# Kernel optimization log

Measured on AMD Instinct MI355X. Metric: run time of the kernel, lower is better.

Reference implementation:

```python
import jax, jax.numpy as jnp
import numpy as np

EPS = 1e-7
B, N, DIM, NH, HD, WIN, HASH_WIN = 2, 1024, 512, 8, 64, 64, 8


def expmap0(v, c):
    sqrt_c = jnp.clip(jnp.sqrt(c), EPS)
    v_norm = jnp.linalg.norm(v, axis=-1, keepdims=True)
    is_zero = v_norm < EPS
    safe = jnp.clip(v_norm, EPS)
    mag = jnp.tanh(sqrt_c * safe) / sqrt_c
    return jnp.where(is_zero, jnp.zeros_like(v), mag * (v / safe))


def poincare_dist(x, y, c):
    # x: (B,H,N,1,D), y: (B,H,N,W,D), c: (B,1,1,1,1) -> (B,H,N,W)
    sqrt_c = jnp.clip(jnp.sqrt(c), EPS)
    x2 = jnp.sum(x * x, -1, keepdims=True)
    y2 = jnp.sum(y * y, -1, keepdims=True)
    xy = jnp.sum(x * y, -1, keepdims=True)
    num = (1 - 2 * c * xy + c * y2) * x + (1 - c * x2) * (-y)
    den = 1 - 2 * c * xy + c * c * x2 * y2
    diff = num / jnp.clip(den, EPS)
    dn = jnp.linalg.norm(diff, axis=-1)
    arg = jnp.minimum(jnp.squeeze(sqrt_c, -1) * jnp.clip(dn, EPS), 1.0 - EPS)
    return 2.0 * jnp.arctanh(arg) / jnp.squeeze(sqrt_c, -1)


def sliding_windows(t, w):
    # t: (B,H,N,D) -> (B,H,N,w,D), left-padded causal window
    Bb, H, Nn, D = t.shape
    pad = jnp.zeros((Bb, H, w - 1, D), t.dtype)
    tp = jnp.concatenate([pad, t], axis=2)
    idx = jnp.arange(w)[None, :] + jnp.arange(Nn)[:, None]  # (N,w)
    return tp[:, :, idx, :]


def layernorm(x, s, b):
    m = jnp.mean(x, -1, keepdims=True)
    v = jnp.var(x, -1, keepdims=True)
    return (x - m) / jnp.sqrt(v + 1e-6) * s + b


def rope(x, cos, sin):
    # x: (B,N,H,hd), cos/sin: (N, hd//2) -- complex rotation in real arithmetic
    xr, xi = jnp.split(x, 2, axis=-1)
    cos = cos[None, :, None, :]
    sin = sin[None, :, None, :]
    return jnp.concatenate([xr * cos - xi * sin, xr * sin + xi * cos], axis=-1)


def setup_inputs() -> dict:
    key = jax.random.key(0)
    ks = jax.random.split(key, 10)
    x = jax.random.normal(ks[0], (B, N, DIM), jnp.float32)
    pos = jnp.arange(N, dtype=jnp.float32)
    inv = 1.0 / (10000.0 ** (jnp.arange(0, HD, 2, dtype=jnp.float32) / HD))
    ang = pos[:, None] * inv[None, :]  # (N, HD//2)
    freqs_cos, freqs_sin = jnp.cos(ang), jnp.sin(ang)
    c = jax.random.uniform(ks[1], (B,), jnp.float32) * 0.9 + 0.1
    s = 0.02
    Wq = jax.random.normal(ks[2], (DIM, DIM), jnp.float32) * s
    Wk = jax.random.normal(ks[3], (DIM, DIM), jnp.float32) * s
    Wv = jax.random.normal(ks[4], (DIM, DIM), jnp.float32) * s
    Wo = jax.random.normal(ks[5], (DIM, DIM), jnp.float32) * s
    W1 = jax.random.normal(ks[6], (DIM, 4 * DIM), jnp.float32) * s
    W2 = jax.random.normal(ks[7], (4 * DIM, DIM), jnp.float32) * s
    bq = jnp.zeros((DIM,)); bk = jnp.zeros((DIM,)); bv = jnp.zeros((DIM,))
    bo = jnp.zeros((DIM,)); b1 = jnp.zeros((4 * DIM,)); b2 = jnp.zeros((DIM,))
    ln1_s = jnp.ones((DIM,)); ln1_b = jnp.zeros((DIM,))
    ln2_s = jnp.ones((DIM,)); ln2_b = jnp.zeros((DIM,))
    geo_scale = jnp.ones((NH, 1, 1), jnp.float32)
    hash_offset = jax.random.normal(ks[8], (1, 1, NH, HD), jnp.float32) * 0.01
    return dict(x=x, freqs_cos=freqs_cos, freqs_sin=freqs_sin, c=c,
                Wq=Wq, bq=bq, Wk=Wk, bk=bk, Wv=Wv, bv=bv, Wo=Wo, bo=bo,
                W1=W1, b1=b1, W2=W2, b2=b2,
                ln1_s=ln1_s, ln1_b=ln1_b, ln2_s=ln2_s, ln2_b=ln2_b,
                geo_scale=geo_scale, hash_offset=hash_offset)


def reference(x, freqs_cos, freqs_sin, c, Wq, bq, Wk, bk, Wv, bv, Wo, bo,
              W1, b1, W2, b2, ln1_s, ln1_b, ln2_s, ln2_b, geo_scale, hash_offset):
    x_res = x
    xn = layernorm(x, ln1_s, ln1_b)
    q = (xn @ Wq + bq).reshape(B, N, NH, HD)
    k = (xn @ Wk + bk).reshape(B, N, NH, HD)
    v = (xn @ Wv + bv).reshape(B, N, NH, HD)
    q = q + hash_offset * jnp.log(1.0 + HASH_WIN)
    q_rot = rope(q, freqs_cos, freqs_sin)
    k_rot = rope(k, freqs_cos, freqs_sin)
    c_b = c.reshape(B, 1, 1, 1)
    q_h = expmap0(q_rot, c_b)
    k_h = expmap0(k_rot, c_b)
    q_h, k_h, v = (t.transpose(0, 2, 1, 3) for t in (q_h, k_h, v))  # (B,H,N,D)
    k_win = sliding_windows(k_h, WIN)  # (B,H,N,W,D)
    v_win = sliding_windows(v, WIN)
    dist = poincare_dist(q_h[:, :, :, None, :], k_win, c.reshape(B, 1, 1, 1, 1))  # (B,H,N,W)
    scores = -geo_scale * dist
    w = jax.nn.softmax(scores, axis=-1)
    attn = jnp.einsum('bhnw,bhnwd->bhnd', w, v_win)
    attn = attn.transpose(0, 2, 1, 3).reshape(B, N, DIM)
    x_out = x_res + (attn @ Wo + bo)
    h = layernorm(x_out, ln2_s, ln2_b)
    ffn = jax.nn.gelu(h @ W1 + b1) @ W2 + b2
    return x_out + ffn
```

## Files before the change

kernel.cpp:

```cpp
#include <hip/hip_runtime.h>
#include <math.h>
#include <stdint.h>

#define Bn   2
#define Nn   1024
#define DIMn 512
#define NHn  8
#define HDn  64
#define QKVS 1536
#define EPSF 1e-7f

typedef __attribute__((ext_vector_type(8))) short short8;
typedef __attribute__((ext_vector_type(4))) float floatx4;
typedef __attribute__((ext_vector_type(4))) float fx4;
typedef __attribute__((ext_vector_type(4))) unsigned short usx4;

__device__ __forceinline__ unsigned short f2bf(float f) {
  union { float f; uint32_t u; } v; v.f = f;
  uint32_t u = v.u;
  return (unsigned short)((u + 0x7FFFu + ((u >> 16) & 1u)) >> 16);
}
__device__ __forceinline__ float bf2f(unsigned short h) {
  union { uint32_t u; float f; } v; v.u = ((uint32_t)h) << 16;
  return v.f;
}

__device__ __forceinline__ float wsum(float v) {
#pragma unroll
  for (int m = 32; m >= 1; m >>= 1) v += __shfl_xor(v, m, 64);
  return v;
}

__device__ __forceinline__ float gelu_tanh(float x) {
  const float k0 = 0.7978845608028654f;
  float x3 = x * x * x;
  return 0.5f * x * (1.f + tanhf(k0 * (x + 0.044715f * x3)));
}

__device__ __forceinline__ void glds16(const unsigned short* g, unsigned short* l) {
  __builtin_amdgcn_global_load_lds((const __attribute__((address_space(1))) void*)g,
                                   (__attribute__((address_space(3))) void*)l, 16, 0, 0);
}

__global__ __launch_bounds__(256) void prep_kernel(
    const float* __restrict__ Wq, const float* __restrict__ Wk,
    const float* __restrict__ Wv, const float* __restrict__ Wo,
    const float* __restrict__ W1, const float* __restrict__ W2,
    unsigned short* __restrict__ Wcat_hi, unsigned short* __restrict__ Wcat_lo,
    unsigned short* __restrict__ Wo_t, unsigned short* __restrict__ W1_t,
    unsigned short* __restrict__ W2_t,
    const float* __restrict__ bq, const float* __restrict__ bk,
    const float* __restrict__ bv, float* __restrict__ bias_cat,
    const float* __restrict__ x, const float* __restrict__ ln1s,
    const float* __restrict__ ln1b,
    unsigned short* __restrict__ xn_hi, unsigned short* __restrict__ xn_lo) {
  __shared__ float t[32][33];
  __shared__ float red[2][4];
  int bid = blockIdx.x;
  int tid = threadIdx.x;
  if (bid == 3072) {
    for (int i = tid; i < 512; i += 256) {
      bias_cat[i] = bq[i];
      bias_cat[512 + i] = bk[i];
      bias_cat[1024 + i] = bv[i];
    }
    return;
  }
  if (bid > 3072) {
    int row = bid - 3073;
    const float* xr = x + (size_t)row * DIMn;
    float2 xv = *(const float2*)(xr + tid * 2);
    float s  = xv.x + xv.y;
    float s2 = xv.x * xv.x + xv.y * xv.y;
    s = wsum(s); s2 = wsum(s2);
    int wv = tid >> 6;
    if ((tid & 63) == 0) { red[0][wv] = s; red[1][wv] = s2; }
    __syncthreads();
    s  = red[0][0] + red[0][1] + red[0][2] + red[0][3];
    s2 = red[1][0] + red[1][1] + red[1][2] + red[1][3];
    float mean = s * (1.f / DIMn);
    float var  = s2 * (1.f / DIMn) - mean * mean;
    float rstd = rsqrtf(var + 1e-6f);
    int d = tid * 2;
    float2 gv = *(const float2*)(ln1s + d);
    float2 bv2 = *(const float2*)(ln1b + d);
    float o0 = (xv.x - mean) * rstd * gv.x + bv2.x;
    float o1 = (xv.y - mean) * rstd * gv.y + bv2.y;
    size_t idx = (size_t)row * DIMn + d;
    unsigned short h0 = f2bf(o0), h1 = f2bf(o1);
    ushort2 hv; hv.x = h0; hv.y = h1;
    *(ushort2*)(xn_hi + idx) = hv;
    ushort2 lv; lv.x = f2bf(o0 - bf2f(h0)); lv.y = f2bf(o1 - bf2f(h1));
    *(ushort2*)(xn_lo + idx) = lv;
    return;
  }
  const float* W;
  unsigned short* hi;
  unsigned short* lo = nullptr;
  int K, N, tix;
  if (bid < 256)       { W = Wq; hi = Wcat_hi;               lo = Wcat_lo;               K = 512;  N = 512;  tix = bid; }
  else if (bid < 512)  { W = Wk; hi = Wcat_hi + 512 * 512;   lo = Wcat_lo + 512 * 512;   K = 512;  N = 512;  tix = bid - 256; }
  else if (bid < 768)  { W = Wv; hi = Wcat_hi + 1024 * 512;  K = 512;  N = 512;  tix = bid - 512; }
  else if (bid < 1024) { W = Wo; hi = Wo_t;                  K = 512;  N = 512;  tix = bid - 768; }
  else if (bid < 2048) { W = W1; hi = W1_t;                  K = 512;  N = 2048; tix = bid - 1024; }
  else                 { W = W2; hi = W2_t;                  K = 2048; N = 512;  tix = bid - 2048; }
  int ntn = N >> 5;
  int kt = tix / ntn, nt = tix - kt * ntn;
  int k0 = kt * 32, n0 = nt * 32;
  {
    int r = tid >> 3, c = (tid & 7) << 2;
    fx4 v = *(const fx4*)&W[(size_t)(k0 + r) * N + n0 + c];
    t[r][c] = v.x; t[r][c + 1] = v.y; t[r][c + 2] = v.z; t[r][c + 3] = v.w;
  }
  __syncthreads();
  for (int i = tid; i < 1024; i += 256) {
    int r = i >> 5, c = i & 31;
    float v = t[c][r];
    unsigned short h = f2bf(v);
    size_t oi = (size_t)(n0 + r) * K + k0 + c;
    hi[oi] = h;
    if (lo) lo[oi] = f2bf(v - bf2f(h));
  }
}

__global__ __launch_bounds__(256) void ln_kernel(const float* __restrict__ x,
                                                 const float* __restrict__ g,
                                                 const float* __restrict__ be,
                                                 unsigned short* __restrict__ yhi) {
  __shared__ float red[2][4];
  int row = blockIdx.x;
  int tid = threadIdx.x;
  const float* xr = x + (size_t)row * DIMn;
  float2 xv = *(const float2*)(xr + tid * 2);
  float s  = xv.x + xv.y;
  float s2 = xv.x * xv.x + xv.y * xv.y;
  s = wsum(s); s2 = wsum(s2);
  int wv = tid >> 6;
  if ((tid & 63) == 0) { red[0][wv] = s; red[1][wv] = s2; }
  __syncthreads();
  s  = red[0][0] + red[0][1] + red[0][2] + red[0][3];
  s2 = red[1][0] + red[1][1] + red[1][2] + red[1][3];
  float mean = s * (1.f / DIMn);
  float var  = s2 * (1.f / DIMn) - mean * mean;
  float rstd = rsqrtf(var + 1e-6f);
  int d = tid * 2;
  float2 gv = *(const float2*)(g + d);
  float2 bv = *(const float2*)(be + d);
  float o0 = (xv.x - mean) * rstd * gv.x + bv.x;
  float o1 = (xv.y - mean) * rstd * gv.y + bv.y;
  size_t idx = (size_t)row * DIMn + d;
  ushort2 hv; hv.x = f2bf(o0); hv.y = f2bf(o1);
  *(ushort2*)(yhi + idx) = hv;
}

template <int BM, int BN, int BKT, int EPI, int OUTBF16>
__global__ __launch_bounds__(256) void gemm_db(
    const unsigned short* __restrict__ Ahi,
    const unsigned short* __restrict__ Bhi,
    const float* __restrict__ bias, const float* __restrict__ res,
    void* __restrict__ outp, int M, int N, int K) {
  constexpr int FI = BM / 32, FJ = BN / 32;
  constexpr int AE = BM * BKT, BE = BN * BKT;
  constexpr int CPR = BKT / 8;
  constexpr int ACH = BM * CPR, BCH = BN * CPR;
  constexpr int CST = BN + 4;
  constexpr int STG = AE + BE;
  constexpr int SMEM_EPI = BM * CST * 2;
  constexpr int SMEM_N = (2 * STG > SMEM_EPI) ? 2 * STG : SMEM_EPI;
  __shared__ __align__(16) unsigned short smem[SMEM_N];

  int tid = threadIdx.x;
  int lane = tid & 63;
  int wid = tid >> 6;
  int wm = (wid >> 1) * (BM / 2), wn = (wid & 1) * (BN / 2);
  int bm = blockIdx.y * BM, bn = blockIdx.x * BN;
  int m16 = lane & 15, kg = lane >> 4;

  floatx4 acc[FI][FJ];
#pragma unroll
  for (int i = 0; i < FI; ++i)
#pragma unroll
    for (int j = 0; j < FJ; ++j) { floatx4 z = {0.f, 0.f, 0.f, 0.f}; acc[i][j] = z; }

  const unsigned short* aph = Ahi + (size_t)bm * K;
  const unsigned short* bph = Bhi + (size_t)bn * K;

  auto stage = [&](int k0, unsigned short* As, unsigned short* Bs) {
    for (int c = tid; c < ACH; c += 256) {
      int row = c / CPR, ci = c % CPR;
      int sci = ci ^ (row & 7);
      glds16(aph + (size_t)row * K + k0 + sci * 8, As + c * 8);
    }
    for (int c = tid; c < BCH; c += 256) {
      int row = c / CPR, ci = c % CPR;
      int sci = ci ^ (row & 7);
      glds16(bph + (size_t)row * K + k0 + sci * 8, Bs + c * 8);
    }
  };

  const int NT = K / BKT;
  stage(0, smem, smem + AE);
  __syncthreads();
  int cur = 0;
  for (int t = 0; t < NT; ++t) {
    unsigned short* As = smem + cur * STG;
    unsigned short* Bs = As + AE;
    int nxt = cur ^ 1;
    if (t + 1 < NT) stage((t + 1) * BKT, smem + nxt * STG, smem + nxt * STG + AE);
#pragma unroll
    for (int ks = 0; ks < BKT / 32; ++ks) {
      short8 ah[FI], bh[FJ];
#pragma unroll
      for (int i = 0; i < FI; ++i) {
        int r = wm + i * 16 + m16;
        ah[i] = *(const short8*)&As[r * BKT + (((ks * 4 + kg) ^ (r & 7)) << 3)];
      }
#pragma unroll
      for (int j = 0; j < FJ; ++j) {
        int r = wn + j * 16 + m16;
        bh[j] = *(const short8*)&Bs[r * BKT + (((ks * 4 + kg) ^ (r & 7)) << 3)];
      }
#pragma unroll
      for (int i = 0; i < FI; ++i)
#pragma unroll
        for (int j = 0; j < FJ; ++j)
          acc[i][j] = __builtin_amdgcn_mfma_f32_16x16x32_bf16(ah[i], bh[j], acc[i][j], 0, 0, 0);
    }
    __syncthreads();
    cur = nxt;
  }

  float* Cs = (float*)smem;
#pragma unroll
  for (int i = 0; i < FI; ++i)
#pragma unroll
    for (int j = 0; j < FJ; ++j)
#pragma unroll
      for (int r = 0; r < 4; ++r)
        Cs[(wm + i * 16 + kg * 4 + r) * CST + wn + j * 16 + m16] = acc[i][j][r];
  __syncthreads();
  constexpr int TOT = BM * BN / 4;
  for (int t = tid; t < TOT; t += 256) {
    int row = (t << 2) / BN;
    int col = (t << 2) & (BN - 1);
    fx4 v = *(const fx4*)&Cs[row * CST + col];
    fx4 bs = *(const fx4*)&bias[bn + col];
    v = v + bs;
    size_t gidx = (size_t)(bm + row) * N + bn + col;
    if constexpr (EPI == 1) {
      fx4 rr = *(const fx4*)&res[gidx];
      v = v + rr;
    }
    if constexpr (EPI == 2) {
      v.x = gelu_tanh(v.x); v.y = gelu_tanh(v.y);
      v.z = gelu_tanh(v.z); v.w = gelu_tanh(v.w);
    }
    if constexpr (OUTBF16) {
      usx4 h;
      h.x = f2bf(v.x); h.y = f2bf(v.y); h.z = f2bf(v.z); h.w = f2bf(v.w);
      *(usx4*)((unsigned short*)outp + gidx) = h;
    } else {
      *(fx4*)((float*)outp + gidx) = v;
    }
  }
}

__global__ __launch_bounds__(256) void qkv_gemm(
    const unsigned short* __restrict__ Ahi, const unsigned short* __restrict__ Alo,
    const unsigned short* __restrict__ Bhi, const unsigned short* __restrict__ Blo,
    const float* __restrict__ bias, float* __restrict__ outp) {
  constexpr int BM = 64, BN = 64, BKT = 32, K = 512, N = QKVS;
  constexpr int FI = 2, FJ = 2;
  constexpr int AE = BM * BKT, BE = BN * BKT;
  constexpr int CST = BN + 4;
  constexpr int STG = 2 * (AE + BE);
  constexpr int SMEM_EPI = BM * CST * 2;
  constexpr int SMEM_N = (2 * STG > SMEM_EPI) ? 2 * STG : SMEM_EPI;
  __shared__ __align__(16) unsigned short smem[SMEM_N];

  int tid = threadIdx.x;
  int lane = tid & 63;
  int wid = tid >> 6;
  int wm = (wid >> 1) * 32, wn = (wid & 1) * 32;
  int bm = blockIdx.y * BM, bn = blockIdx.x * BN;
  int m16 = lane & 15, kg = lane >> 4;
  bool dos = bn < 1024;

  floatx4 acc[FI][FJ];
#pragma unroll
  for (int i = 0; i < FI; ++i)
#pragma unroll
    for (int j = 0; j < FJ; ++j) { floatx4 z = {0.f, 0.f, 0.f, 0.f}; acc[i][j] = z; }

  const unsigned short* aph = Ahi + (size_t)bm * K;
  const unsigned short* bph = Bhi + (size_t)bn * K;
  const unsigned short* apl = Alo + (size_t)bm * K;
  const unsigned short* bpl = Blo + (size_t)bn * K;

  auto stage = [&](int k0, unsigned short* buf) {
    {
      int c = tid;
      int row = c >> 2, ci = c & 3;
      int sci = ci ^ ((row >> 1) & 3);
      glds16(aph + (size_t)row * K + k0 + sci * 8, buf + c * 8);
      if (dos) glds16(apl + (size_t)row * K + k0 + sci * 8, buf + AE + c * 8);
    }
    {
      int c = tid;
      int row = c >> 2, ci = c & 3;
      int sci = ci ^ ((row >> 1) & 3);
      glds16(bph + (size_t)row * K + k0 + sci * 8, buf + 2 * AE + c * 8);
      if (dos) glds16(bpl + (size_t)row * K + k0 + sci * 8, buf + 2 * AE + BE + c * 8);
    }
  };

  const int NT = K / BKT;
  stage(0, smem);
  __syncthreads();
  int cur = 0;
  for (int t = 0; t < NT; ++t) {
    unsigned short* buf = smem + cur * STG;
    unsigned short* AsHi = buf;
    unsigned short* AsLo = buf + AE;
    unsigned short* BsHi = buf + 2 * AE;
    unsigned short* BsLo = buf + 2 * AE + BE;
    int nxt = cur ^ 1;
    if (t + 1 < NT) stage((t + 1) * BKT, smem + nxt * STG);

    short8 ah[FI], bh[FJ], al[FI], bl[FJ];
#pragma unroll
    for (int i = 0; i < FI; ++i) {
      int r = wm + i * 16 + m16;
      int off = r * BKT + ((kg ^ ((r >> 1) & 3)) << 3);
      ah[i] = *(const short8*)&AsHi[off];
      if (dos) al[i] = *(const short8*)&AsLo[off];
    }
#pragma unroll
    for (int j = 0; j < FJ; ++j) {
      int r = wn + j * 16 + m16;
      int off = r * BKT + ((kg ^ ((r >> 1) & 3)) << 3);
      bh[j] = *(const short8*)&BsHi[off];
      if (dos) bl[j] = *(const short8*)&BsLo[off];
    }
#pragma unroll
    for (int i = 0; i < FI; ++i)
#pragma unroll
      for (int j = 0; j < FJ; ++j) {
        acc[i][j] = __builtin_amdgcn_mfma_f32_16x16x32_bf16(ah[i], bh[j], acc[i][j], 0, 0, 0);
        if (dos) {
          acc[i][j] = __builtin_amdgcn_mfma_f32_16x16x32_bf16(al[i], bh[j], acc[i][j], 0, 0, 0);
          acc[i][j] = __builtin_amdgcn_mfma_f32_16x16x32_bf16(ah[i], bl[j], acc[i][j], 0, 0, 0);
        }
      }
    __syncthreads();
    cur = nxt;
  }

  float* Cs = (float*)smem;
#pragma unroll
  for (int i = 0; i < FI; ++i)
#pragma unroll
    for (int j = 0; j < FJ; ++j)
#pragma unroll
      for (int r = 0; r < 4; ++r)
        Cs[(wm + i * 16 + kg * 4 + r) * CST + wn + j * 16 + m16] = acc[i][j][r];
  __syncthreads();
  constexpr int TOT = BM * BN / 4;
  for (int t = tid; t < TOT; t += 256) {
    int row = (t << 2) / BN;
    int col = (t << 2) & (BN - 1);
    fx4 v = *(const fx4*)&Cs[row * CST + col];
    fx4 bs = *(const fx4*)&bias[bn + col];
    v = v + bs;
    size_t gidx = (size_t)(bm + row) * N + bn + col;
    *(fx4*)(outp + gidx) = v;
  }
}

__global__ __launch_bounds__(512) void attn_fused(const float* __restrict__ qkv,
                                                  const float* __restrict__ fcos,
                                                  const float* __restrict__ fsin,
                                                  const float* __restrict__ cvec,
                                                  const float* __restrict__ geo,
                                                  const float* __restrict__ hash,
                                                  unsigned short* __restrict__ attn_out) {
  __shared__ unsigned short Qhi[32][72], Qlo[32][72];
  __shared__ unsigned short Khi[96][72], Klo[96][72];
  __shared__ unsigned short Vt[64][104];
  __shared__ unsigned short Pb[32][104];
  __shared__ float Sf[32][97];
  __shared__ float x2s[32], bxs[32], y2s[96], gys[96];

  int tid = threadIdx.x, lane = tid & 63, wv = tid >> 6;
  int bid = blockIdx.x;
  int nt = bid & 31, h = (bid >> 5) & 7, b = bid >> 8;
  int n0 = nt * 32;
  float c = cvec[b];
  float sqc = sqrtf(c);
  float rsqc = 1.f / sqc;
  float gs = geo[h];
  int dr = lane & 31;
  bool hih = lane >= 32;
  const float LOG9 = 2.1972245773362196f;
  float hofr = hash[h * HDn + dr] * LOG9;
  float hofi = hash[h * HDn + dr + 32] * LOG9;

  for (int i = tid; i < 32 * 52; i += 512) ((uint32_t*)Pb)[i] = 0u;

#pragma unroll
  for (int i = 0; i < 4; ++i) {
    int q = wv * 4 + i;
    int n = n0 + q;
    size_t bas = (size_t)(b * Nn + n) * QKVS + h * HDn;
    float qr = qkv[bas + dr] + hofr;
    float qi = qkv[bas + dr + 32] + hofi;
    float cs = fcos[n * 32 + dr], sn = fsin[n * 32 + dr];
    float qv = hih ? (qr * sn + qi * cs) : (qr * cs - qi * sn);
    float nq = sqrtf(wsum(qv * qv));
    float sq = fmaxf(nq, EPSF);
    float t = sqc * sq;
    float em = expf(-2.f * t);
    float opem = 1.f + em;
    float mag = ((1.f - em) / opem) * rsqc;
    float sech2 = 4.f * em / (opem * opem);
    float oq = (nq < EPSF) ? 0.f : mag * (qv / sq);
    unsigned short hh = f2bf(oq);
    Qhi[q][lane] = hh;
    Qlo[q][lane] = f2bf(oq - bf2f(hh));
    if (lane == 0) {
      x2s[q] = (nq < EPSF) ? 0.f : mag * mag;
      bxs[q] = (nq < EPSF) ? 1.f : sech2;
    }
  }
#pragma unroll 4
  for (int i = 0; i < 12; ++i) {
    int r = wv * 12 + i;
    int gi = n0 - 64 + r;
    float ok = 0.f, vf = 0.f, y2 = 0.f, gy = 1.f;
    if (gi >= 0) {
      size_t bas = (size_t)(b * Nn + gi) * QKVS + h * HDn;
      float kr = qkv[bas + 512 + dr];
      float ki = qkv[bas + 512 + dr + 32];
      vf = qkv[bas + 1024 + lane];
      float cs = fcos[gi * 32 + dr], sn = fsin[gi * 32 + dr];
      float kv = hih ? (kr * sn + ki * cs) : (kr * cs - ki * sn);
      float nk = sqrtf(wsum(kv * kv));
      float sk = fmaxf(nk, EPSF);
      float t = sqc * sk;
      float em = expf(-2.f * t);
      float opem = 1.f + em;
      float mag = ((1.f - em) / opem) * rsqc;
      float sech2 = 4.f * em / (opem * opem);
      ok = (nk < EPSF) ? 0.f : mag * (kv / sk);
      y2 = (nk < EPSF) ? 0.f : mag * mag;
      gy = (nk < EPSF) ? 1.f : sech2;
    }
    unsigned short hh = f2bf(ok);
    Khi[r][lane] = hh;
    Klo[r][lane] = f2bf(ok - bf2f(hh));
    Vt[lane][r] = f2bf(vf);
    if (lane == 0) { y2s[r] = y2; gys[r] = gy; }
  }
  __syncthreads();

  int m16 = lane & 15, kg = lane >> 4;
#pragma unroll
  for (int uu = 0; uu < 2; ++uu) {
    int u = wv + uu * 8;
    if (u < 12) {
      int mt = u / 6, ntile = u % 6;
      floatx4 acc = {0.f, 0.f, 0.f, 0.f};
#pragma unroll
      for (int ks = 0; ks < 2; ++ks) {
        short8 ah = *(const short8*)&Qhi[mt * 16 + m16][ks * 32 + kg * 8];
        short8 al = *(const short8*)&Qlo[mt * 16 + m16][ks * 32 + kg * 8];
        short8 bh = *(const short8*)&Khi[ntile * 16 + m16][ks * 32 + kg * 8];
        short8 bl = *(const short8*)&Klo[ntile * 16 + m16][ks * 32 + kg * 8];
        acc = __builtin_amdgcn_mfma_f32_16x16x32_bf16(ah, bh, acc, 0, 0, 0);
        acc = __builtin_amdgcn_mfma_f32_16x16x32_bf16(al, bh, acc, 0, 0, 0);
        acc = __builtin_amdgcn_mfma_f32_16x16x32_bf16(ah, bl, acc, 0, 0, 0);
      }
#pragma unroll
      for (int r = 0; r < 4; ++r) Sf[mt * 16 + kg * 4 + r][ntile * 16 + m16] = acc[r];
    }
  }
  __syncthreads();

#pragma unroll
  for (int i = 0; i < 4; ++i) {
    int nl = wv * 4 + i;
    int r = nl + 1 + lane;
    float xy = Sf[nl][r];
    float x2 = x2s[nl], y2 = y2s[r];
    float bx = bxs[nl], gy = gys[r];

    float den = fmaf(c * c * x2, y2, fmaf(-2.f * c, xy, 1.f));
    den = fmaxf(den, EPSF);
    float rden = 1.f / den;
    float s2 = fmaxf(x2 - 2.f * xy + y2, 0.f);
    float z = sqrtf(c * s2 * rden);
    float omz2 = bx * gy * rden;
    float opz = 1.f + fminf(z, 1.f);
    float ratio = fminf(opz * opz / omz2, 1.9999999e7f);
    float sc = -gs * logf(ratio) * rsqc;

    float e = expf(sc);
    float se = wsum(e);
    Pb[nl][r] = f2bf(e / se);
  }
  __syncthreads();

  {
    int mt = wv >> 2, ntile = wv & 3;
    floatx4 acc = {0.f, 0.f, 0.f, 0.f};
#pragma unroll
    for (int ks = 0; ks < 3; ++ks) {
      short8 a = *(const short8*)&Pb[mt * 16 + m16][ks * 32 + kg * 8];
      short8 bb = *(const short8*)&Vt[ntile * 16 + m16][ks * 32 + kg * 8];
      acc = __builtin_amdgcn_mfma_f32_16x16x32_bf16(a, bb, acc, 0, 0, 0);
    }
#pragma unroll
    for (int r = 0; r < 4; ++r) {
      int qrow = mt * 16 + kg * 4 + r;
      int d = ntile * 16 + m16;
      attn_out[(size_t)(b * Nn + n0 + qrow) * DIMn + h * HDn + d] = f2bf(acc[r]);
    }
  }
}

extern "C" void kernel_launch(void* const* d_in, const int* in_sizes, int n_in,
                              void* d_out, int out_size, void* d_ws, size_t ws_size,
                              hipStream_t stream) {
  const float* x    = (const float*)d_in[0];
  const float* fcos = (const float*)d_in[1];
  const float* fsin = (const float*)d_in[2];
  const float* cvec = (const float*)d_in[3];
  const float* Wq = (const float*)d_in[4];  const float* bq = (const float*)d_in[5];
  const float* Wk = (const float*)d_in[6];  const float* bk = (const float*)d_in[7];
  const float* Wv = (const float*)d_in[8];  const float* bv = (const float*)d_in[9];
  const float* Wo = (const float*)d_in[10]; const float* bo = (const float*)d_in[11];
  const float* W1 = (const float*)d_in[12]; const float* b1 = (const float*)d_in[13];
  const float* W2 = (const float*)d_in[14]; const float* b2 = (const float*)d_in[15];
  const float* ln1s = (const float*)d_in[16]; const float* ln1b = (const float*)d_in[17];
  const float* ln2s = (const float*)d_in[18]; const float* ln2b = (const float*)d_in[19];
  const float* geo  = (const float*)d_in[20]; const float* hash = (const float*)d_in[21];
  float* out = (float*)d_out;
  char* base = (char*)d_ws;

  unsigned short* Wcat_hi = (unsigned short*)(base + 0);
  unsigned short* Wcat_lo = (unsigned short*)(base + 1572864);
  unsigned short* Wo_t    = (unsigned short*)(base + 3145728);
  unsigned short* W1_t    = (unsigned short*)(base + 3670016);
  unsigned short* W2_t    = (unsigned short*)(base + 5767168);
  unsigned short* xn_hi   = (unsigned short*)(base + 7864320);
  unsigned short* xn_lo   = (unsigned short*)(base + 9961472);
  float*          qkv     = (float*)(base + 12058624);
  unsigned short* attnb   = (unsigned short*)(base + 7864320);
  float*          xout    = (float*)(base + 9961472);
  unsigned short* hbuf    = (unsigned short*)(base + 14155776);
  unsigned short* mid     = (unsigned short*)(base + 16252928);
  float*          bias_cat= (float*)(base + 24641536);

  const int M = Bn * Nn;

  prep_kernel<<<3073 + M, 256, 0, stream>>>(Wq, Wk, Wv, Wo, W1, W2, Wcat_hi, Wcat_lo,
                                            Wo_t, W1_t, W2_t, bq, bk, bv, bias_cat,
                                            x, ln1s, ln1b, xn_hi, xn_lo);
  qkv_gemm<<<dim3(QKVS / 64, M / 64), 256, 0, stream>>>(
      xn_hi, xn_lo, Wcat_hi, Wcat_lo, bias_cat, qkv);
  attn_fused<<<Bn * NHn * (Nn / 32), 512, 0, stream>>>(qkv, fcos, fsin, cvec, geo, hash, attnb);
  gemm_db<32, 32, 64, 1, 0><<<dim3(DIMn / 32, M / 32), 256, 0, stream>>>(
      attnb, Wo_t, bo, x, xout, M, DIMn, 512);
  ln_kernel<<<M, 256, 0, stream>>>(xout, ln2s, ln2b, hbuf);
  gemm_db<64, 64, 64, 2, 1><<<dim3(2048 / 64, M / 64), 256, 0, stream>>>(
      hbuf, W1_t, b1, nullptr, mid, M, 2048, 512);
  gemm_db<32, 32, 64, 1, 0><<<dim3(DIMn / 32, M / 32), 256, 0, stream>>>(
      mid, W2_t, b2, xout, out, M, DIMn, 2048);
}
```

Baseline: 179.9 us.

## Move Wo/W1/W2 transposes into QKV GEMM launch and use 64x64 transpose tiles

The weight transpose and bf16 conversion of Wo, W1 and W2 moves out of the prep kernel into extra blocks appended to the QKV GEMM grid. Those blocks overlap with the GEMM and shorten the critical prep kernel, which now handles only Wq/Wk/Wv and the first layernorm. Transposes now use 64x64 tiles with vectorized 4-wide bf16 stores, replacing 32x32 tiles with scalar stores. The QKV GEMM grid becomes 1D with a manual block index decode, and its shared memory is reused as the transpose tile, which must be large enough.

Result: no change. 179.9 us (median of 2 runs) (+0.0%).

```diff
diff --git a/kernel.cpp b/kernel.cpp
--- a/kernel.cpp
+++ b/kernel.cpp
@@ -42,23 +42,67 @@
                                    (__attribute__((address_space(3))) void*)l, 16, 0, 0);
 }
 
+__device__ void tr64(const float* __restrict__ W, unsigned short* __restrict__ hi,
+                     unsigned short* __restrict__ lo, int K, int N, int tix, int tid,
+                     float* tile ) {
+  int ntn = N >> 6;
+  int kt = tix / ntn, nt = tix - kt * ntn;
+  int k0 = kt * 64, n0 = nt * 64;
+  int rb = tid >> 4, c4 = (tid & 15) * 4;
+#pragma unroll
+  for (int rr = 0; rr < 4; ++rr) {
+    int r = rr * 16 + rb;
+    fx4 v = *(const fx4*)&W[(size_t)(k0 + r) * N + n0 + c4];
+    tile[r * 65 + c4] = v.x;
+    tile[r * 65 + c4 + 1] = v.y;
+    tile[r * 65 + c4 + 2] = v.z;
+    tile[r * 65 + c4 + 3] = v.w;
+  }
+  __syncthreads();
+#pragma unroll
+  for (int rr = 0; rr < 4; ++rr) {
+    int r = rr * 16 + rb;
+    usx4 hv, lv;
+#pragma unroll
+    for (int j = 0; j < 4; ++j) {
+      float v = tile[(c4 + j) * 65 + r];
+      unsigned short h = f2bf(v);
+      hv[j] = h;
+      lv[j] = f2bf(v - bf2f(h));
+    }
+    size_t oi = (size_t)(n0 + r) * K + k0 + c4;
+    *(usx4*)&hi[oi] = hv;
+    if (lo) *(usx4*)&lo[oi] = lv;
+  }
+  __syncthreads();
+}
+
 __global__ __launch_bounds__(256) void prep_kernel(
     const float* __restrict__ Wq, const float* __restrict__ Wk,
-    const float* __restrict__ Wv, const float* __restrict__ Wo,
-    const float* __restrict__ W1, const float* __restrict__ W2,
+    const float* __restrict__ Wv,
     unsigned short* __restrict__ Wcat_hi, unsigned short* __restrict__ Wcat_lo,
-    unsigned short* __restrict__ Wo_t, unsigned short* __restrict__ W1_t,
-    unsigned short* __restrict__ W2_t,
     const float* __restrict__ bq, const float* __restrict__ bk,
     const float* __restrict__ bv, float* __restrict__ bias_cat,
     const float* __restrict__ x, const float* __restrict__ ln1s,
     const float* __restrict__ ln1b,
     unsigned short* __restrict__ xn_hi, unsigned short* __restrict__ xn_lo) {
-  __shared__ float t[32][33];
+  __shared__ float tile[64 * 65];
   __shared__ float red[2][4];
   int bid = blockIdx.x;
   int tid = threadIdx.x;
-  if (bid == 3072) {
+  if (bid < 64) {
+    tr64(Wq, Wcat_hi, Wcat_lo, 512, 512, bid, tid, tile);
+    return;
+  }
+  if (bid < 128) {
+    tr64(Wk, Wcat_hi + 512 * 512, Wcat_lo + 512 * 512, 512, 512, bid - 64, tid, tile);
+    return;
+  }
+  if (bid < 192) {
+    tr64(Wv, Wcat_hi + 1024 * 512, nullptr, 512, 512, bid - 128, tid, tile);
+    return;
+  }
+  if (bid == 192) {
     for (int i = tid; i < 512; i += 256) {
       bias_cat[i] = bq[i];
       bias_cat[512 + i] = bk[i];
@@ -66,61 +110,31 @@
     }
     return;
   }
-  if (bid > 3072) {
-    int row = bid - 3073;
-    const float* xr = x + (size_t)row * DIMn;
-    float2 xv = *(const float2*)(xr + tid * 2);
-    float s  = xv.x + xv.y;
-    float s2 = xv.x * xv.x + xv.y * xv.y;
-    s = wsum(s); s2 = wsum(s2);
-    int wv = tid >> 6;
-    if ((tid & 63) == 0) { red[0][wv] = s; red[1][wv] = s2; }
-    __syncthreads();
-    s  = red[0][0] + red[0][1] + red[0][2] + red[0][3];
-    s2 = red[1][0] + red[1][1] + red[1][2] + red[1][3];
-    float mean = s * (1.f / DIMn);
-    float var  = s2 * (1.f / DIMn) - mean * mean;
-    float rstd = rsqrtf(var + 1e-6f);
-    int d = tid * 2;
-    float2 gv = *(const float2*)(ln1s + d);
-    float2 bv2 = *(const float2*)(ln1b + d);
-    float o0 = (xv.x - mean) * rstd * gv.x + bv2.x;
-    float o1 = (xv.y - mean) * rstd * gv.y + bv2.y;
-    size_t idx = (size_t)row * DIMn + d;
-    unsigned short h0 = f2bf(o0), h1 = f2bf(o1);
-    ushort2 hv; hv.x = h0; hv.y = h1;
-    *(ushort2*)(xn_hi + idx) = hv;
-    ushort2 lv; lv.x = f2bf(o0 - bf2f(h0)); lv.y = f2bf(o1 - bf2f(h1));
-    *(ushort2*)(xn_lo + idx) = lv;
-    return;
-  }
-  const float* W;
-  unsigned short* hi;
-  unsigned short* lo = nullptr;
-  int K, N, tix;
-  if (bid < 256)       { W = Wq; hi = Wcat_hi;               lo = Wcat_lo;               K = 512;  N = 512;  tix = bid; }
-  else if (bid < 512)  { W = Wk; hi = Wcat_hi + 512 * 512;   lo = Wcat_lo + 512 * 512;   K = 512;  N = 512;  tix = bid - 256; }
-  else if (bid < 768)  { W = Wv; hi = Wcat_hi + 1024 * 512;  K = 512;  N = 512;  tix = bid - 512; }
-  else if (bid < 1024) { W = Wo; hi = Wo_t;                  K = 512;  N = 512;  tix = bid - 768; }
-  else if (bid < 2048) { W = W1; hi = W1_t;                  K = 512;  N = 2048; tix = bid - 1024; }
-  else                 { W = W2; hi = W2_t;                  K = 2048; N = 512;  tix = bid - 2048; }
-  int ntn = N >> 5;
-  int kt = tix / ntn, nt = tix - kt * ntn;
-  int k0 = kt * 32, n0 = nt * 32;
-  {
-    int r = tid >> 3, c = (tid & 7) << 2;
-    fx4 v = *(const fx4*)&W[(size_t)(k0 + r) * N + n0 + c];
-    t[r][c] = v.x; t[r][c + 1] = v.y; t[r][c + 2] = v.z; t[r][c + 3] = v.w;
-  }
-  __syncthreads();
-  for (int i = tid; i < 1024; i += 256) {
-    int r = i >> 5, c = i & 31;
-    float v = t[c][r];
-    unsigned short h = f2bf(v);
-    size_t oi = (size_t)(n0 + r) * K + k0 + c;
-    hi[oi] = h;
-    if (lo) lo[oi] = f2bf(v - bf2f(h));
-  }
+  int row = bid - 193;
+  const float* xr = x + (size_t)row * DIMn;
+  float2 xv = *(const float2*)(xr + tid * 2);
+  float s  = xv.x + xv.y;
+  float s2 = xv.x * xv.x + xv.y * xv.y;
+  s = wsum(s); s2 = wsum(s2);
+  int wv = tid >> 6;
+  if ((tid & 63) == 0) { red[0][wv] = s; red[1][wv] = s2; }
+  __syncthreads();
+  s  = red[0][0] + red[0][1] + red[0][2] + red[0][3];
+  s2 = red[1][0] + red[1][1] + red[1][2] + red[1][3];
+  float mean = s * (1.f / DIMn);
+  float var  = s2 * (1.f / DIMn) - mean * mean;
+  float rstd = rsqrtf(var + 1e-6f);
+  int d = tid * 2;
+  float2 gv = *(const float2*)(ln1s + d);
+  float2 bv2 = *(const float2*)(ln1b + d);
+  float o0 = (xv.x - mean) * rstd * gv.x + bv2.x;
+  float o1 = (xv.y - mean) * rstd * gv.y + bv2.y;
+  size_t idx = (size_t)row * DIMn + d;
+  unsigned short h0 = f2bf(o0), h1 = f2bf(o1);
+  ushort2 hv; hv.x = h0; hv.y = h1;
+  *(ushort2*)(xn_hi + idx) = hv;
+  ushort2 lv; lv.x = f2bf(o0 - bf2f(h0)); lv.y = f2bf(o1 - bf2f(h1));
+  *(ushort2*)(xn_lo + idx) = lv;
 }
 
 __global__ __launch_bounds__(256) void ln_kernel(const float* __restrict__ x,
@@ -268,7 +282,11 @@
 __global__ __launch_bounds__(256) void qkv_gemm(
     const unsigned short* __restrict__ Ahi, const unsigned short* __restrict__ Alo,
     const unsigned short* __restrict__ Bhi, const unsigned short* __restrict__ Blo,
-    const float* __restrict__ bias, float* __restrict__ outp) {
+    const float* __restrict__ bias, float* __restrict__ outp,
+    const float* __restrict__ Wo, const float* __restrict__ W1,
+    const float* __restrict__ W2,
+    unsigned short* __restrict__ Wo_t, unsigned short* __restrict__ W1_t,
+    unsigned short* __restrict__ W2_t) {
   constexpr int BM = 64, BN = 64, BKT = 32, K = 512, N = QKVS;
   constexpr int FI = 2, FJ = 2;
   constexpr int AE = BM * BKT, BE = BN * BKT;
@@ -279,10 +297,21 @@
   __shared__ __align__(16) unsigned short smem[SMEM_N];
 
   int tid = threadIdx.x;
+  int bid = blockIdx.x;
+
+  if (bid >= 768) {
+    float* tile = (float*)smem;
+    int tix = bid - 768;
+    if (tix < 64)       tr64(Wo, Wo_t, nullptr, 512, 512, tix, tid, tile);
+    else if (tix < 320) tr64(W1, W1_t, nullptr, 512, 2048, tix - 64, tid, tile);
+    else                tr64(W2, W2_t, nullptr, 2048, 512, tix - 320, tid, tile);
+    return;
+  }
+
   int lane = tid & 63;
   int wid = tid >> 6;
   int wm = (wid >> 1) * 32, wn = (wid & 1) * 32;
-  int bm = blockIdx.y * BM, bn = blockIdx.x * BN;
+  int bm = (bid / 24) * BM, bn = (bid % 24) * BN;
   int m16 = lane & 15, kg = lane >> 4;
   bool dos = bn < 1024;
 
@@ -563,11 +592,12 @@
 
   const int M = Bn * Nn;
 
-  prep_kernel<<<3073 + M, 256, 0, stream>>>(Wq, Wk, Wv, Wo, W1, W2, Wcat_hi, Wcat_lo,
-                                            Wo_t, W1_t, W2_t, bq, bk, bv, bias_cat,
-                                            x, ln1s, ln1b, xn_hi, xn_lo);
-  qkv_gemm<<<dim3(QKVS / 64, M / 64), 256, 0, stream>>>(
-      xn_hi, xn_lo, Wcat_hi, Wcat_lo, bias_cat, qkv);
+  prep_kernel<<<193 + M, 256, 0, stream>>>(Wq, Wk, Wv, Wcat_hi, Wcat_lo,
+                                           bq, bk, bv, bias_cat,
+                                           x, ln1s, ln1b, xn_hi, xn_lo);
+  qkv_gemm<<<768 + 576, 256, 0, stream>>>(
+      xn_hi, xn_lo, Wcat_hi, Wcat_lo, bias_cat, qkv,
+      Wo, W1, W2, Wo_t, W1_t, W2_t);
   attn_fused<<<Bn * NHn * (Nn / 32), 512, 0, stream>>>(qkv, fcos, fsin, cvec, geo, hash, attnb);
   gemm_db<32, 32, 64, 1, 0><<<dim3(DIMn / 32, M / 32), 256, 0, stream>>>(
       attnb, Wo_t, bo, x, xout, M, DIMn, 512);
```
